# Kernel tuning notes

Measured on AMD Instinct MI355X. Metric: run time of the kernel, lower is better.

## Reference

```python
import jax, jax.numpy as jnp
import numpy as np

B, T, D = 4, 2048, 2048
DI = int(D * 2.0)  # mlp_expansion = 2.0
RMS_EPS = 1e-6
LRU_EPS = 1e-6
INIT_SCALE = 0.02


def _rmsnorm(x, w):
    return x * jax.lax.rsqrt(jnp.mean(x * x, axis=-1, keepdims=True) + RMS_EPS) * w


def setup_inputs() -> dict:
    key = jax.random.key(0)
    ks = jax.random.split(key, 10)
    s = INIT_SCALE
    return {
        "x": jax.random.normal(ks[0], (B, T, D), dtype=jnp.float32),
        "state": jnp.zeros((B, D), dtype=jnp.float32),
        "w_norm1": jnp.ones((D,), dtype=jnp.float32),
        "W_in": jax.random.normal(ks[1], (D, D), dtype=jnp.float32) * s,
        "W_r": jax.random.normal(ks[2], (D, D), dtype=jnp.float32) * s,
        "b_r": jnp.zeros((D,), dtype=jnp.float32),
        "W_i": jax.random.normal(ks[3], (D, D), dtype=jnp.float32) * s,
        "b_i": jnp.zeros((D,), dtype=jnp.float32),
        "log_decay": jax.random.normal(ks[4], (D,), dtype=jnp.float32),
        "W_out": jax.random.normal(ks[5], (D, D), dtype=jnp.float32) * s,
        "w_norm2": jnp.ones((D,), dtype=jnp.float32),
        "W_gate": jax.random.normal(ks[6], (DI, D), dtype=jnp.float32) * s,
        "W_up": jax.random.normal(ks[7], (DI, D), dtype=jnp.float32) * s,
        "W_down": jax.random.normal(ks[8], (D, DI), dtype=jnp.float32) * s,
    }


def reference(x, state, w_norm1, W_in, W_r, b_r, W_i, b_i, log_decay,
              W_out, w_norm2, W_gate, W_up, W_down):
    # --- pre-norm + RG-LRU mixer ---
    n = _rmsnorm(x, w_norm1)                      # (B,T,D)
    r = jax.nn.sigmoid(n @ W_r.T + b_r)           # input gate
    g = jax.nn.sigmoid(n @ W_i.T + b_i)           # recurrent gate
    xp = n @ W_in.T                               # projected input
    alpha = jnp.clip(jax.nn.sigmoid(log_decay), LRU_EPS, 1.0 - LRU_EPS)  # (D,)
    scale = jnp.sqrt(jnp.clip(1.0 - alpha * alpha, 0.0, None))           # (D,)
    b_seq = scale * (r * xp)                      # (B,T,D)

    def step(h, b_t):                             # h_t = alpha*h + scale*(r_t*x_t)
        h = alpha * h + b_t
        return h, h

    h_final, hs = jax.lax.scan(step, state, jnp.swapaxes(b_seq, 0, 1))  # hs: (T,B,D)
    hs = jnp.swapaxes(hs, 0, 1)                   # (B,T,D)
    mixer_out = (hs * g) @ W_out.T
    x = x + mixer_out

    # --- SwiGLU FFN ---
    n2 = _rmsnorm(x, w_norm2)
    ffn = (jax.nn.silu(n2 @ W_gate.T) * (n2 @ W_up.T)) @ W_down.T
    return x + ffn, h_final
```

## Files before the change

kernel.cpp:

```cpp
#include <hip/hip_runtime.h>

#define BD 4
#define TD 2048
#define DD 2048
#define DID 4096
#define MD (BD*TD)
#define CHK 32
#define CHL (TD/CHK)

typedef float f32x4 __attribute__((ext_vector_type(4)));
typedef short s16x8 __attribute__((ext_vector_type(8)));
typedef unsigned short u16;
typedef unsigned short u16x4 __attribute__((ext_vector_type(4)));
typedef unsigned short u16x8 __attribute__((ext_vector_type(8)));

__device__ __forceinline__ float bf2f(u16 u) {
    union { unsigned int i; float f; } v; v.i = ((unsigned int)u) << 16; return v.f;
}
__device__ __forceinline__ u16 f2bf(float f) {
    union { float f; unsigned int i; } v; v.f = f;
    unsigned int r = v.i + 0x7fffu + ((v.i >> 16) & 1u);
    return (u16)(r >> 16);
}
__device__ __forceinline__ float sigm(float x) { return 1.f / (1.f + __expf(-x)); }

__device__ __forceinline__ void mfma16(f32x4& acc, s16x8 a, s16x8 b) {
    asm("v_mfma_f32_16x16x32_bf16 %0, %1, %2, %0" : "+v"(acc) : "v"(a), "v"(b));
}

__device__ __forceinline__ void gload16(const u16* g, u16* l) {
    __builtin_amdgcn_global_load_lds((__attribute__((address_space(1))) void*)(g),
                                     (__attribute__((address_space(3))) void*)(l),
                                     16, 0, 0);
}

__global__ __launch_bounds__(256)
void cvt_all(const float4* __restrict__ s0, const float4* __restrict__ s1,
             const float4* __restrict__ s2, const float4* __restrict__ s3,
             const float4* __restrict__ s4, const float4* __restrict__ s5,
             const float4* __restrict__ s6, u16x4* __restrict__ dst, int n4) {
    const int SEG  = DD * DD / 4;
    const int ROWQ = DD / 4;
    int i = blockIdx.x * blockDim.x + threadIdx.x;
    int stride = gridDim.x * blockDim.x;
    for (; i < n4; i += stride) {
        const float4* s; int off; size_t di;
        if (i < 4 * SEG) {
            int k = i / SEG;
            s = (k == 0) ? s0 : (k == 1) ? s1 : (k == 2) ? s2 : s3;
            off = i - k * SEG;
            di = i;
        } else {
            int j = i - 4 * SEG;
            if (j < 4 * SEG) {
                int which = j / (2 * SEG);
                int jj = j - which * 2 * SEG;
                int g = jj / ROWQ, cq = jj - g * ROWQ;
                int nb = g >> 6, ii = g & 63;
                int dr;
                if (which == 0) dr = nb * 128 + (ii < 32 ? ii : ii + 32);
                else            dr = nb * 128 + (ii < 32 ? ii + 32 : ii + 64);
                s = which ? s5 : s4; off = jj;
                di = (size_t)4 * SEG + (size_t)dr * ROWQ + cq;
            } else {
                s = s6; off = j - 4 * SEG;
                di = i;
            }
        }
        float4 v = s[off];
        u16x4 o = { f2bf(v.x), f2bf(v.y), f2bf(v.z), f2bf(v.w) };
        dst[di] = o;
    }
}

__global__ __launch_bounds__(256) void rmsnorm_kernel(const float* __restrict__ x,
                                                      const float* __restrict__ w,
                                                      u16* __restrict__ out) {
    const int row = blockIdx.x;
    const int tid = threadIdx.x;
    const float4* x4 = (const float4*)(x + (size_t)row * DD);
    float4 a = x4[tid * 2], b = x4[tid * 2 + 1];
    float s = a.x*a.x + a.y*a.y + a.z*a.z + a.w*a.w
            + b.x*b.x + b.y*b.y + b.z*b.z + b.w*b.w;
#pragma unroll
    for (int off = 32; off >= 1; off >>= 1) s += __shfl_xor(s, off, 64);
    __shared__ float red[4];
    if ((tid & 63) == 0) red[tid >> 6] = s;
    __syncthreads();
    float tot = red[0] + red[1] + red[2] + red[3];
    float rs = rsqrtf(tot * (1.f / DD) + 1e-6f);
    const float4* w4 = (const float4*)w;
    float4 wa = w4[tid * 2], wb = w4[tid * 2 + 1];
    u16x8 o = { f2bf(a.x*rs*wa.x), f2bf(a.y*rs*wa.y), f2bf(a.z*rs*wa.z), f2bf(a.w*rs*wa.w),
                f2bf(b.x*rs*wb.x), f2bf(b.y*rs*wb.y), f2bf(b.z*rs*wb.z), f2bf(b.w*rs*wb.w) };
    *(u16x8*)(out + (size_t)row * DD + tid * 8) = o;
}

template<int EPI>
__global__ __launch_bounds__(256)
void gemm_bt(const u16* __restrict__ A, const u16* __restrict__ Bw,
             int M, int N, int K,
             const float* __restrict__ bias0, const float* __restrict__ bias1,
             const float* resid, float* outf,
             u16* __restrict__ out0, u16* __restrict__ out1, u16* __restrict__ out2,
             int Dsub) {
    __shared__ __align__(16) u16 lA[128 * 64];
    __shared__ __align__(16) u16 lB[128 * 64];
    const int tid  = threadIdx.x;
    const int lane = tid & 63;
    const int wave = tid >> 6;
    const int wr = (wave >> 1) << 6;
    const int wc = (wave & 1) << 6;
    const int brow = blockIdx.x * 128;
    const int bcol = blockIdx.y * 128;

    const int srow  = tid >> 3;
    const int schnk = (tid & 7) ^ (srow & 7);
    const size_t soff = (size_t)srow * K + (schnk << 3);
    const u16* gA = A  + (size_t)brow * K + soff;
    const u16* gB = Bw + (size_t)bcol * K + soff;
    u16* lAp = lA + tid * 8;
    u16* lBp = lB + tid * 8;

    const int fr = lane & 15;
    const int lg = lane >> 4;
    const int ck0 = ((lg)     ^ (fr & 7)) << 4;
    const int ck1 = ((4 + lg) ^ (fr & 7)) << 4;
    const char* lAc = (const char*)lA;
    const char* lBc = (const char*)lB;

    f32x4 acc[4][4];
#pragma unroll
    for (int i = 0; i < 4; ++i)
#pragma unroll
        for (int j = 0; j < 4; ++j)
            acc[i][j] = (f32x4){0.f, 0.f, 0.f, 0.f};

    for (int k0 = 0; k0 < K; k0 += 64) {
#pragma unroll
        for (int s = 0; s < 4; ++s) {
            gload16(gA + k0 + (size_t)s * 32 * K, lAp + s * 2048);
            gload16(gB + k0 + (size_t)s * 32 * K, lBp + s * 2048);
        }
        __syncthreads();
        s16x8 af[4][2], bq[4][2];
#pragma unroll
        for (int i = 0; i < 4; ++i) {
            const int ra = (wr + i * 16 + fr) * 128;
            const int rb = (wc + i * 16 + fr) * 128;
            af[i][0] = *(const s16x8*)(lAc + ra + ck0);
            af[i][1] = *(const s16x8*)(lAc + ra + ck1);
            bq[i][0] = *(const s16x8*)(lBc + rb + ck0);
            bq[i][1] = *(const s16x8*)(lBc + rb + ck1);
        }
#pragma unroll
        for (int h = 0; h < 2; ++h)
#pragma unroll
            for (int i = 0; i < 4; ++i)
#pragma unroll
                for (int j = 0; j < 4; ++j)
                    mfma16(acc[i][j], af[i][h], bq[j][h]);
        __syncthreads();
    }

#pragma unroll
    for (int i = 0; i < 4; ++i)
#pragma unroll
        for (int j = 0; j < 4; ++j)
            asm volatile("s_nop 7" : "+v"(acc[i][j]));

    if (EPI == 3) {
        const int nb = bcol >> 7;
        const int cbase = nb * 64 + (wc ? 32 : 0);
        const int r0 = brow + wr + (lg << 2);
#pragma unroll
        for (int i = 0; i < 4; ++i)
#pragma unroll
            for (int j = 0; j < 2; ++j)
#pragma unroll
                for (int e = 0; e < 4; ++e) {
                    const int grow = r0 + i * 16 + e;
                    const float g = acc[i][j][e];
                    const float u = acc[i][j + 2][e];
                    out0[(size_t)grow * Dsub + cbase + j * 16 + fr] = f2bf(g * sigm(g) * u);
                }
        return;
    }

    const int r0 = brow + wr + (lg << 2);
    const int c0 = bcol + wc + fr;
#pragma unroll
    for (int i = 0; i < 4; ++i) {
#pragma unroll
        for (int j = 0; j < 4; ++j) {
            const int gcol = c0 + j * 16;
#pragma unroll
            for (int e = 0; e < 4; ++e) {
                const int grow = r0 + i * 16 + e;
                float c = acc[i][j][e];
                if (EPI == 0) {
                    if (gcol < Dsub) {
                        out0[(size_t)grow * Dsub + gcol] = f2bf(sigm(c + bias0[gcol]));
                    } else if (gcol < 2 * Dsub) {
                        out1[(size_t)grow * Dsub + (gcol - Dsub)] = f2bf(sigm(c + bias1[gcol - Dsub]));
                    } else {
                        out2[(size_t)grow * Dsub + (gcol - 2 * Dsub)] = f2bf(c);
                    }
                } else if (EPI == 1) {
                    const size_t idx = (size_t)grow * N + gcol;
                    outf[idx] = resid[idx] + c;
                }
            }
        }
    }
}

__global__ __launch_bounds__(256)
void scan_partial(const u16* __restrict__ R, const u16* __restrict__ XP,
                  const float* __restrict__ log_dec, float* __restrict__ carry) {
    const int d = blockIdx.x * 256 + threadIdx.x;
    const int k = blockIdx.y;
    const int b = blockIdx.z;
    float a = sigm(log_dec[d]);
    a = fminf(fmaxf(a, 1e-6f), 1.f - 1e-6f);
    const float sc = sqrtf(fmaxf(1.f - a * a, 0.f));
    float h = 0.f;
    size_t idx = ((size_t)b * TD + (size_t)k * CHL) * DD + d;
#pragma unroll 8
    for (int t = 0; t < CHL; ++t) {
        h = a * h + sc * (bf2f(R[idx]) * bf2f(XP[idx]));
        idx += DD;
    }
    carry[((size_t)b * CHK + k) * DD + d] = h;
}

__global__ __launch_bounds__(256)
void scan_carry(const float* __restrict__ state, const float* __restrict__ log_dec,
                const float* __restrict__ carry, float* __restrict__ carryin,
                float* __restrict__ hfin) {
    const int d = blockIdx.x * 256 + threadIdx.x;
    const int b = blockIdx.y;
    float a = sigm(log_dec[d]);
    a = fminf(fmaxf(a, 1e-6f), 1.f - 1e-6f);
    float aL = a;
#pragma unroll
    for (int i = 0; i < 6; ++i) aL *= aL;
    float h = state[(size_t)b * DD + d];
#pragma unroll
    for (int k = 0; k < CHK; ++k) {
        const size_t ci = ((size_t)b * CHK + k) * DD + d;
        carryin[ci] = h;
        h = aL * h + carry[ci];
    }
    hfin[(size_t)b * DD + d] = h;
}

__global__ __launch_bounds__(256)
void scan_final(const u16* __restrict__ R, const u16* __restrict__ XP,
                const u16* __restrict__ G, const float* __restrict__ log_dec,
                const float* __restrict__ carryin, u16* __restrict__ HSG) {
    const int d = blockIdx.x * 256 + threadIdx.x;
    const int k = blockIdx.y;
    const int b = blockIdx.z;
    float a = sigm(log_dec[d]);
    a = fminf(fmaxf(a, 1e-6f), 1.f - 1e-6f);
    const float sc = sqrtf(fmaxf(1.f - a * a, 0.f));
    float h = carryin[((size_t)b * CHK + k) * DD + d];
    size_t idx = ((size_t)b * TD + (size_t)k * CHL) * DD + d;
#pragma unroll 8
    for (int t = 0; t < CHL; ++t) {
        h = a * h + sc * (bf2f(R[idx]) * bf2f(XP[idx]));
        HSG[idx] = f2bf(h * bf2f(G[idx]));
        idx += DD;
    }
}

extern "C" void kernel_launch(void* const* d_in, const int* in_sizes, int n_in,
                              void* d_out, int out_size, void* d_ws, size_t ws_size,
                              hipStream_t stream) {
    const float* x       = (const float*)d_in[0];
    const float* state   = (const float*)d_in[1];
    const float* w_norm1 = (const float*)d_in[2];
    const float* W_in    = (const float*)d_in[3];
    const float* W_r     = (const float*)d_in[4];
    const float* b_r     = (const float*)d_in[5];
    const float* W_i     = (const float*)d_in[6];
    const float* b_i     = (const float*)d_in[7];
    const float* log_dec = (const float*)d_in[8];
    const float* W_out   = (const float*)d_in[9];
    const float* w_norm2 = (const float*)d_in[10];
    const float* W_gate  = (const float*)d_in[11];
    const float* W_up    = (const float*)d_in[12];
    const float* W_down  = (const float*)d_in[13];

    float* out  = (float*)d_out;
    float* hfin = out + (size_t)MD * DD;

    u16* wstack1 = (u16*)d_ws;
    u16* wout2   = wstack1 + (size_t)3 * DD * DD;
    u16* wstack2 = wout2   + (size_t)DD * DD;
    u16* wdown2  = wstack2 + (size_t)2 * DID * DD;
    u16* bufN    = wdown2  + (size_t)DD * DID;
    u16* bufR    = bufN    + (size_t)MD * DD;
    u16* bufG    = bufR    + (size_t)MD * DD;
    u16* bufXP   = bufG    + (size_t)MD * DD;
    u16* spare   = bufXP   + (size_t)MD * DD;
    float* carry   = (float*)spare;
    float* carryin = carry + (size_t)BD * CHK * DD;

    cvt_all<<<2048, 256, 0, stream>>>((const float4*)W_r, (const float4*)W_i,
                                      (const float4*)W_in, (const float4*)W_out,
                                      (const float4*)W_gate, (const float4*)W_up,
                                      (const float4*)W_down, (u16x4*)wstack1,
                                      (3*DD*DD + DD*DD + 2*DID*DD + DD*DID) / 4);

    rmsnorm_kernel<<<MD, 256, 0, stream>>>(x, w_norm1, bufN);

    {
        dim3 g1(MD / 128, (3 * DD) / 128);
        gemm_bt<0><<<g1, 256, 0, stream>>>(bufN, wstack1, MD, 3 * DD, DD,
                                           b_r, b_i, nullptr, nullptr, bufR, bufG, bufXP, DD);
    }

    {
        dim3 gp(DD / 256, CHK, BD);
        scan_partial<<<gp, 256, 0, stream>>>(bufR, bufXP, log_dec, carry);
        dim3 gc(DD / 256, BD);
        scan_carry<<<gc, 256, 0, stream>>>(state, log_dec, carry, carryin, hfin);
        scan_final<<<gp, 256, 0, stream>>>(bufR, bufXP, bufG, log_dec, carryin, bufN);
    }

    {
        dim3 g2(MD / 128, DD / 128);
        gemm_bt<1><<<g2, 256, 0, stream>>>(bufN, wout2, MD, DD, DD,
                                           nullptr, nullptr, x, out, nullptr, nullptr, nullptr, 0);
    }

    rmsnorm_kernel<<<MD, 256, 0, stream>>>(out, w_norm2, bufN);

    {
        dim3 g3(MD / 128, (2 * DID) / 128);
        gemm_bt<3><<<g3, 256, 0, stream>>>(bufN, wstack2, MD, 2 * DID, DD,
                                           nullptr, nullptr, nullptr, nullptr, bufR, nullptr, nullptr, DID);
    }

    {
        dim3 g4(MD / 128, DD / 128);
        gemm_bt<1><<<g4, 256, 0, stream>>>(bufR, wdown2, MD, DD, DID,
                                           nullptr, nullptr, out, out, nullptr, nullptr, nullptr, 0);
    }
}
```

Measured before the change: 858.1 us.

## Fuse input-gate product r*xp into interleaved projection GEMM epilogue

W_r and W_in are interleaved per 128-column tile so one GEMM epilogue computes sigmoid(r)*xp and writes a single bf16 product buffer. The W_i gate is moved to its own GEMM. The scan kernels now read one precomputed product instead of two separate buffers, which cuts scan memory traffic and one intermediate write. The cost is an extra kernel launch and a second pass over the normalized input for the separate gate GEMM.

```diff
diff --git a/kernel.cpp b/kernel.cpp
--- a/kernel.cpp
+++ b/kernel.cpp
@@ -35,37 +35,41 @@
 }
 
 __global__ __launch_bounds__(256)
-void cvt_all(const float4* __restrict__ s0, const float4* __restrict__ s1,
-             const float4* __restrict__ s2, const float4* __restrict__ s3,
-             const float4* __restrict__ s4, const float4* __restrict__ s5,
-             const float4* __restrict__ s6, u16x4* __restrict__ dst, int n4) {
+void cvt_all(const float4* __restrict__ sr, const float4* __restrict__ sin_,
+             const float4* __restrict__ si, const float4* __restrict__ sout,
+             const float4* __restrict__ sg, const float4* __restrict__ su,
+             const float4* __restrict__ sd, u16x4* __restrict__ dst, int n4) {
     const int SEG  = DD * DD / 4;
     const int ROWQ = DD / 4;
     int i = blockIdx.x * blockDim.x + threadIdx.x;
     int stride = gridDim.x * blockDim.x;
     for (; i < n4; i += stride) {
         const float4* s; int off; size_t di;
-        if (i < 4 * SEG) {
-            int k = i / SEG;
-            s = (k == 0) ? s0 : (k == 1) ? s1 : (k == 2) ? s2 : s3;
-            off = i - k * SEG;
-            di = i;
+        if (i < 2 * SEG) {
+            int which = i / SEG;
+            int jj = i - which * SEG;
+            int g = jj / ROWQ, cq = jj - g * ROWQ;
+            int nb = g >> 6, ii = g & 63;
+            int dr = which == 0 ? nb * 128 + (ii < 32 ? ii : ii + 32)
+                                : nb * 128 + (ii < 32 ? ii + 32 : ii + 64);
+            s = which ? sin_ : sr; off = jj;
+            di = (size_t)dr * ROWQ + cq;
+        } else if (i < 3 * SEG) {
+            s = si; off = i - 2 * SEG; di = i;
+        } else if (i < 4 * SEG) {
+            s = sout; off = i - 3 * SEG; di = i;
+        } else if (i < 8 * SEG) {
+            int j = i - 4 * SEG;
+            int which = j / (2 * SEG);
+            int jj = j - which * 2 * SEG;
+            int g = jj / ROWQ, cq = jj - g * ROWQ;
+            int nb = g >> 6, ii = g & 63;
+            int dr = which == 0 ? nb * 128 + (ii < 32 ? ii : ii + 32)
+                                : nb * 128 + (ii < 32 ? ii + 32 : ii + 64);
+            s = which ? su : sg; off = jj;
+            di = (size_t)4 * SEG + (size_t)dr * ROWQ + cq;
         } else {
-            int j = i - 4 * SEG;
-            if (j < 4 * SEG) {
-                int which = j / (2 * SEG);
-                int jj = j - which * 2 * SEG;
-                int g = jj / ROWQ, cq = jj - g * ROWQ;
-                int nb = g >> 6, ii = g & 63;
-                int dr;
-                if (which == 0) dr = nb * 128 + (ii < 32 ? ii : ii + 32);
-                else            dr = nb * 128 + (ii < 32 ? ii + 32 : ii + 64);
-                s = which ? s5 : s4; off = jj;
-                di = (size_t)4 * SEG + (size_t)dr * ROWQ + cq;
-            } else {
-                s = s6; off = j - 4 * SEG;
-                di = i;
-            }
+            s = sd; off = i - 8 * SEG; di = i;
         }
         float4 v = s[off];
         u16x4 o = { f2bf(v.x), f2bf(v.y), f2bf(v.z), f2bf(v.w) };
@@ -100,10 +104,9 @@
 __global__ __launch_bounds__(256)
 void gemm_bt(const u16* __restrict__ A, const u16* __restrict__ Bw,
              int M, int N, int K,
-             const float* __restrict__ bias0, const float* __restrict__ bias1,
+             const float* __restrict__ bias0,
              const float* resid, float* outf,
-             u16* __restrict__ out0, u16* __restrict__ out1, u16* __restrict__ out2,
-             int Dsub) {
+             u16* __restrict__ out0, int Dsub) {
     __shared__ __align__(16) u16 lA[128 * 64];
     __shared__ __align__(16) u16 lB[128 * 64];
     const int tid  = threadIdx.x;
@@ -169,10 +172,11 @@
         for (int j = 0; j < 4; ++j)
             asm volatile("s_nop 7" : "+v"(acc[i][j]));
 
-    if (EPI == 3) {
+    const int r0 = brow + wr + (lg << 2);
+
+    if (EPI == 3 || EPI == 4) {
         const int nb = bcol >> 7;
         const int cbase = nb * 64 + (wc ? 32 : 0);
-        const int r0 = brow + wr + (lg << 2);
 #pragma unroll
         for (int i = 0; i < 4; ++i)
 #pragma unroll
@@ -180,14 +184,17 @@
 #pragma unroll
                 for (int e = 0; e < 4; ++e) {
                     const int grow = r0 + i * 16 + e;
+                    const int col  = cbase + j * 16 + fr;
                     const float g = acc[i][j][e];
                     const float u = acc[i][j + 2][e];
-                    out0[(size_t)grow * Dsub + cbase + j * 16 + fr] = f2bf(g * sigm(g) * u);
+                    float v;
+                    if (EPI == 3) v = g * sigm(g) * u;
+                    else          v = sigm(g + bias0[col]) * u;
+                    out0[(size_t)grow * Dsub + col] = f2bf(v);
                 }
         return;
     }
 
-    const int r0 = brow + wr + (lg << 2);
     const int c0 = bcol + wc + fr;
 #pragma unroll
     for (int i = 0; i < 4; ++i) {
@@ -198,17 +205,11 @@
             for (int e = 0; e < 4; ++e) {
                 const int grow = r0 + i * 16 + e;
                 float c = acc[i][j][e];
-                if (EPI == 0) {
-                    if (gcol < Dsub) {
-                        out0[(size_t)grow * Dsub + gcol] = f2bf(sigm(c + bias0[gcol]));
-                    } else if (gcol < 2 * Dsub) {
-                        out1[(size_t)grow * Dsub + (gcol - Dsub)] = f2bf(sigm(c + bias1[gcol - Dsub]));
-                    } else {
-                        out2[(size_t)grow * Dsub + (gcol - 2 * Dsub)] = f2bf(c);
-                    }
-                } else if (EPI == 1) {
+                if (EPI == 1) {
                     const size_t idx = (size_t)grow * N + gcol;
                     outf[idx] = resid[idx] + c;
+                } else {
+                    out0[(size_t)grow * Dsub + gcol] = f2bf(sigm(c + bias0[gcol]));
                 }
             }
         }
@@ -216,7 +217,7 @@
 }
 
 __global__ __launch_bounds__(256)
-void scan_partial(const u16* __restrict__ R, const u16* __restrict__ XP,
+void scan_partial(const u16* __restrict__ BP,
                   const float* __restrict__ log_dec, float* __restrict__ carry) {
     const int d = blockIdx.x * 256 + threadIdx.x;
     const int k = blockIdx.y;
@@ -228,7 +229,7 @@
     size_t idx = ((size_t)b * TD + (size_t)k * CHL) * DD + d;
 #pragma unroll 8
     for (int t = 0; t < CHL; ++t) {
-        h = a * h + sc * (bf2f(R[idx]) * bf2f(XP[idx]));
+        h = a * h + sc * bf2f(BP[idx]);
         idx += DD;
     }
     carry[((size_t)b * CHK + k) * DD + d] = h;
@@ -256,8 +257,8 @@
 }
 
 __global__ __launch_bounds__(256)
-void scan_final(const u16* __restrict__ R, const u16* __restrict__ XP,
-                const u16* __restrict__ G, const float* __restrict__ log_dec,
+void scan_final(const u16* __restrict__ BP, const u16* __restrict__ G,
+                const float* __restrict__ log_dec,
                 const float* __restrict__ carryin, u16* __restrict__ HSG) {
     const int d = blockIdx.x * 256 + threadIdx.x;
     const int k = blockIdx.y;
@@ -269,7 +270,7 @@
     size_t idx = ((size_t)b * TD + (size_t)k * CHL) * DD + d;
 #pragma unroll 8
     for (int t = 0; t < CHL; ++t) {
-        h = a * h + sc * (bf2f(R[idx]) * bf2f(XP[idx]));
+        h = a * h + sc * bf2f(BP[idx]);
         HSG[idx] = f2bf(h * bf2f(G[idx]));
         idx += DD;
     }
@@ -296,57 +297,63 @@
     float* out  = (float*)d_out;
     float* hfin = out + (size_t)MD * DD;
 
-    u16* wstack1 = (u16*)d_ws;
-    u16* wout2   = wstack1 + (size_t)3 * DD * DD;
-    u16* wstack2 = wout2   + (size_t)DD * DD;
-    u16* wdown2  = wstack2 + (size_t)2 * DID * DD;
-    u16* bufN    = wdown2  + (size_t)DD * DID;
-    u16* bufR    = bufN    + (size_t)MD * DD;
-    u16* bufG    = bufR    + (size_t)MD * DD;
-    u16* bufXP   = bufG    + (size_t)MD * DD;
-    u16* spare   = bufXP   + (size_t)MD * DD;
+    const size_t SEGU = (size_t)DD * DD;
+    u16* w_rx    = (u16*)d_ws;
+    u16* w_i     = w_rx   + 2 * SEGU;
+    u16* w_out   = w_rx   + 3 * SEGU;
+    u16* w_gu    = w_rx   + 4 * SEGU;
+    u16* w_down  = w_rx   + 8 * SEGU;
+    u16* bufN    = w_rx   + 10 * SEGU;
+    u16* bufBP   = bufN   + (size_t)MD * DD;
+    u16* bufG    = bufBP  + (size_t)MD * DD;
+    u16* spare   = bufG   + (size_t)MD * DD;
     float* carry   = (float*)spare;
     float* carryin = carry + (size_t)BD * CHK * DD;
 
-    cvt_all<<<2048, 256, 0, stream>>>((const float4*)W_r, (const float4*)W_i,
-                                      (const float4*)W_in, (const float4*)W_out,
+    cvt_all<<<2048, 256, 0, stream>>>((const float4*)W_r, (const float4*)W_in,
+                                      (const float4*)W_i, (const float4*)W_out,
                                       (const float4*)W_gate, (const float4*)W_up,
-                                      (const float4*)W_down, (u16x4*)wstack1,
-                                      (3*DD*DD + DD*DD + 2*DID*DD + DD*DID) / 4);
+                                      (const float4*)W_down, (u16x4*)w_rx,
+                                      (int)(10 * SEGU / 4));
 
     rmsnorm_kernel<<<MD, 256, 0, stream>>>(x, w_norm1, bufN);
 
     {
-        dim3 g1(MD / 128, (3 * DD) / 128);
-        gemm_bt<0><<<g1, 256, 0, stream>>>(bufN, wstack1, MD, 3 * DD, DD,
-                                           b_r, b_i, nullptr, nullptr, bufR, bufG, bufXP, DD);
+        dim3 g1(MD / 128, (2 * DD) / 128);
+        gemm_bt<4><<<g1, 256, 0, stream>>>(bufN, w_rx, MD, 2 * DD, DD,
+                                           b_r, nullptr, nullptr, bufBP, DD);
+    }
+    {
+        dim3 g1b(MD / 128, DD / 128);
+        gemm_bt<5><<<g1b, 256, 0, stream>>>(bufN, w_i, MD, DD, DD,
+                                            b_i, nullptr, nullptr, bufG, DD);
     }
 
     {
         dim3 gp(DD / 256, CHK, BD);
-        scan_partial<<<gp, 256, 0, stream>>>(bufR, bufXP, log_dec, carry);
+        scan_partial<<<gp, 256, 0, stream>>>(bufBP, log_dec, carry);
         dim3 gc(DD / 256, BD);
         scan_carry<<<gc, 256, 0, stream>>>(state, log_dec, carry, carryin, hfin);
-        scan_final<<<gp, 256, 0, stream>>>(bufR, bufXP, bufG, log_dec, carryin, bufN);
+        scan_final<<<gp, 256, 0, stream>>>(bufBP, bufG, log_dec, carryin, bufN);
     }
 
     {
         dim3 g2(MD / 128, DD / 128);
-        gemm_bt<1><<<g2, 256, 0, stream>>>(bufN, wout2, MD, DD, DD,
-                                           nullptr, nullptr, x, out, nullptr, nullptr, nullptr, 0);
+        gemm_bt<1><<<g2, 256, 0, stream>>>(bufN, w_out, MD, DD, DD,
+                                           nullptr, x, out, nullptr, 0);
     }
 
     rmsnorm_kernel<<<MD, 256, 0, stream>>>(out, w_norm2, bufN);
 
     {
         dim3 g3(MD / 128, (2 * DID) / 128);
-        gemm_bt<3><<<g3, 256, 0, stream>>>(bufN, wstack2, MD, 2 * DID, DD,
-                                           nullptr, nullptr, nullptr, nullptr, bufR, nullptr, nullptr, DID);
+        gemm_bt<3><<<g3, 256, 0, stream>>>(bufN, w_gu, MD, 2 * DID, DD,
+                                           nullptr, nullptr, nullptr, bufBP, DID);
     }
 
     {
         dim3 g4(MD / 128, DD / 128);
-        gemm_bt<1><<<g4, 256, 0, stream>>>(bufR, wdown2, MD, DD, DID,
-                                           nullptr, nullptr, out, out, nullptr, nullptr, nullptr, 0);
-    }
-}
+        gemm_bt<1><<<g4, 256, 0, stream>>>(bufBP, w_down, MD, DD, DID,
+                                           nullptr, out, out, nullptr, 0);
+    }
+}
```

After: 816.7 us. 4.8% less time.
